# Optimization experiments

Hardware: AMD Instinct MI355X
Metric: run time of the kernel (lower is better)

## Reference

```python
import jax, jax.numpy as jnp
import numpy as np

AUTHOR_FAMILY_CODET = jnp.array([0, 1, 2, 1, 3, 3], dtype=jnp.int32)
MARGIN = 0.3

def setup_inputs() -> dict:
    key = jax.random.key(0)
    k1, k2 = jax.random.split(key)
    B, D = 8192, 256
    embeddings = jax.random.normal(k1, (B, D), dtype=jnp.float32)
    labels = jax.random.randint(k2, (B,), 0, 6, dtype=jnp.int64)
    return {"embeddings": embeddings, "labels": labels}

def reference(embeddings, labels):
    B = embeddings.shape[0]
    # family lookup; labels out of table range would be -1 (cannot happen here
    # since fill_max == table length, but kept for faithfulness)
    lab = labels.astype(jnp.int32)
    table_len = AUTHOR_FAMILY_CODET.shape[0]
    fam = jnp.where(lab < table_len,
                    AUTHOR_FAMILY_CODET[jnp.clip(lab, 0, table_len - 1)],
                    -1)
    # cosine distance matrix [B, B]
    emb_norm = embeddings / jnp.linalg.norm(embeddings, axis=-1, keepdims=True)
    dist = 1.0 - emb_norm @ emb_norm.T
    valid_row = fam >= 0                                   # [B]
    same = (fam[:, None] == fam[None, :]) & valid_row[:, None]
    same = same & ~jnp.eye(B, dtype=bool)                  # exclude self
    diff = (fam[:, None] != fam[None, :]) & valid_row[None, :] & valid_row[:, None]
    d_pos = jnp.max(jnp.where(same, dist, -2.0), axis=1)   # hardest positive
    d_neg = jnp.min(jnp.where(diff, dist, 4.0), axis=1)    # hardest negative
    valid = valid_row & jnp.any(same, axis=1) & jnp.any(diff, axis=1)
    triplet = jax.nn.relu(d_pos - d_neg + MARGIN) * valid.astype(dist.dtype)
    count = jnp.sum(valid.astype(jnp.int32))
    return jnp.sum(triplet) / jnp.maximum(count, 1).astype(dist.dtype)
```

## Files before the change

### kernel.cpp

```cpp
#include <hip/hip_runtime.h>


typedef __attribute__((ext_vector_type(8))) _Float16 half8;
typedef __attribute__((ext_vector_type(4))) float floatx4;
typedef __attribute__((ext_vector_type(4))) unsigned short ushort4v;

constexpr int D = 256;
#define MARGIN 0.3f
#define FAM_PACKED 111240

static __device__ __forceinline__ void ld_g2l16(const unsigned short* g,
                                                unsigned short* l) {
  __builtin_amdgcn_global_load_lds(
      (const __attribute__((address_space(1))) unsigned int*)(const void*)g,
      (__attribute__((address_space(3))) unsigned int*)(void*)l, 16, 0, 0);
}

static __device__ __forceinline__ unsigned packmm(float mn, float mx) {
  unsigned lo = __builtin_bit_cast(unsigned short, (_Float16)mn);
  unsigned hi = __builtin_bit_cast(unsigned short, (_Float16)mx);
  return lo | (hi << 16);
}
static __device__ __forceinline__ float mmlo(unsigned p) {
  return (float)__builtin_bit_cast(_Float16, (unsigned short)(p & 0xFFFF));
}
static __device__ __forceinline__ float mmhi(unsigned p) {
  return (float)__builtin_bit_cast(_Float16, (unsigned short)(p >> 16));
}

__global__ __launch_bounds__(256) void prep_kernel(
    const float* __restrict__ E, const int* __restrict__ labels,
    unsigned short* __restrict__ Eh, int* __restrict__ fam,
    float* __restrict__ sumAcc, int* __restrict__ cntAcc,
    int* __restrict__ doneCnt, int B) {
  if (blockIdx.x == 0 && threadIdx.x == 0) {
    sumAcc[0] = 0.0f; cntAcc[0] = 0; doneCnt[0] = 0;
  }
  int wave = blockIdx.x * 4 + (threadIdx.x >> 6);
  int lane = threadIdx.x & 63;
  int nw   = gridDim.x * 4;
  for (int row = wave; row < B; row += nw) {
    float4 v = *(const float4*)&E[(long)row * D + lane * 4];
    float s = v.x * v.x + v.y * v.y + v.z * v.z + v.w * v.w;
#pragma unroll
    for (int o = 1; o < 64; o <<= 1) s += __shfl_xor(s, o);
    float rn = 1.0f / sqrtf(s);
    ushort4v o4;
    o4.x = __builtin_bit_cast(unsigned short, (_Float16)(v.x * rn));
    o4.y = __builtin_bit_cast(unsigned short, (_Float16)(v.y * rn));
    o4.z = __builtin_bit_cast(unsigned short, (_Float16)(v.z * rn));
    o4.w = __builtin_bit_cast(unsigned short, (_Float16)(v.w * rn));
    *(ushort4v*)&Eh[(long)row * D + lane * 4] = o4;
    if (lane == 0) {
      int lab = labels[row];
      int labc = lab < 0 ? 0 : (lab > 5 ? 5 : lab);
      fam[row] = (lab < 6) ? ((FAM_PACKED >> (3 * labc)) & 7) : -1;
    }
  }
}

__global__ __launch_bounds__(256) void gram_kernel(
    const unsigned short* __restrict__ Eh, const int* __restrict__ fam,
    unsigned* __restrict__ part, int nt, int nTasks) {
  __shared__ unsigned short Bs[2][64 * 256];
  __shared__ unsigned colS[2][4][64];

  const int tid = threadIdx.x;
  const int w = tid >> 6, l = tid & 63;
  const int m = l & 15, q = l >> 4;
  const int half = w & 1;

  int srcRel[8];
#pragma unroll
  for (int t = 0; t < 8; ++t) {
    int c = w * 512 + t * 64 + l;
    int row = c >> 5, ch = c & 31;
    srcRel[t] = row * D + ((ch ^ (row & 7)) << 3);
  }

  const int t0 = (int)(((long)blockIdx.x * nTasks) / gridDim.x);
  const int t1 = (int)(((long)(blockIdx.x + 1) * nTasks) / gridDim.x);

  int rb = 0;
  while ((rb + 1) * (nt - rb) <= t0) ++rb;
  int ct = 2 * rb + (t0 - rb * (nt - rb + 1));

  half8 apan[8][2];
  int famv;
  {
    const int r0w = rb * 128 + w * 32;
#pragma unroll
    for (int ks = 0; ks < 8; ++ks)
#pragma unroll
      for (int mi = 0; mi < 2; ++mi)
        apan[ks][mi] = *(const half8*)
            &Eh[(long)(r0w + mi * 16 + m) * D + ks * 32 + q * 8];
    famv = fam[r0w + (l & 31)];
  }

  {
    const unsigned short* src = Eh + (long)ct * 64 * D;
#pragma unroll
    for (int t = 0; t < 8; ++t)
      ld_g2l16(src + srcRel[t], &Bs[0][(w * 512 + t * 64) * 8]);
  }

  int p = 0;
  int mct = -1, mrb = -1;
#pragma unroll 1
  for (int f = t0; f < t1; ++f) {
    __syncthreads();

    if (mct >= 0 && l < 16) {
      const int sb = (f - 1) & 1;
      const int col = w * 16 + l;
      float mn = 4.0f, mx = -4.0f;
#pragma unroll
      for (int ww = 0; ww < 4; ++ww) {
        unsigned pk = colS[sb][ww][col];
        mn = fminf(mn, mmlo(pk));
        mx = fmaxf(mx, mmhi(pk));
      }
      part[((long)mct * nt + mrb) * 64 + col] = packmm(mn, mx);
    }

    const int rt64 = 2 * rb + (w >> 1);
    const bool doit = (rt64 <= ct);
    const int sb = f & 1;
    floatx4 acc[2][4];
#pragma unroll
    for (int mi = 0; mi < 2; ++mi)
#pragma unroll
      for (int nj = 0; nj < 4; ++nj) acc[mi][nj] = (floatx4)0.0f;

    if (doit) {
      const unsigned short* bufp = &Bs[p][0];
#pragma unroll
      for (int ks = 0; ks < 8; ++ks) {
        half8 b[4];
#pragma unroll
        for (int nj = 0; nj < 4; ++nj) {
          int row = nj * 16 + m;
          b[nj] = *(const half8*)
              &bufp[row * 256 + (((ks * 4 + q) ^ (m & 7)) << 3)];
        }
#pragma unroll
        for (int mi = 0; mi < 2; ++mi)
#pragma unroll
          for (int nj = 0; nj < 4; ++nj)
            acc[mi][nj] = __builtin_amdgcn_mfma_f32_16x16x32_f16(
                apan[ks][mi], b[nj], acc[mi][nj], 0, 0, 0);
      }
    }

    int nrb = rb, nct = ct + 1;
    if (nct == nt) { ++nrb; nct = 2 * nrb; }
    if (f + 1 < t1) {
      const unsigned short* src = Eh + (long)nct * 64 * D;
#pragma unroll
      for (int t = 0; t < 8; ++t)
        ld_g2l16(src + srcRel[t], &Bs[p ^ 1][(w * 512 + t * 64) * 8]);
    }

    if (doit) {
      const int famcv = fam[ct * 64 + l];
      int famR[8], famC[4];
#pragma unroll
      for (int mi = 0; mi < 2; ++mi)
#pragma unroll
        for (int r = 0; r < 4; ++r)
          famR[mi * 4 + r] = __shfl(famv, mi * 16 + q * 4 + r);
#pragma unroll
      for (int nj = 0; nj < 4; ++nj) famC[nj] = __shfl(famcv, nj * 16 + m);

      float rMin[8], rMax[8], cMin[4], cMax[4];
#pragma unroll
      for (int i = 0; i < 8; ++i) { rMin[i] = 4.0f; rMax[i] = -4.0f; }
#pragma unroll
      for (int j = 0; j < 4; ++j) { cMin[j] = 4.0f; cMax[j] = -4.0f; }

#pragma unroll
      for (int mi = 0; mi < 2; ++mi)
#pragma unroll
        for (int nj = 0; nj < 4; ++nj)
#pragma unroll
          for (int r = 0; r < 4; ++r) {
            float d = acc[mi][nj][r];
            bool same = (famR[mi * 4 + r] == famC[nj]);
            float ds = same ? d : 4.0f;
            float dd = same ? -4.0f : d;
            rMin[mi * 4 + r] = fminf(rMin[mi * 4 + r], ds);
            rMax[mi * 4 + r] = fmaxf(rMax[mi * 4 + r], dd);
            cMin[nj] = fminf(cMin[nj], ds);
            cMax[nj] = fmaxf(cMax[nj], dd);
          }

#pragma unroll
      for (int o = 1; o < 16; o <<= 1)
#pragma unroll
        for (int i = 0; i < 8; ++i) {
          rMin[i] = fminf(rMin[i], __shfl_xor(rMin[i], o));
          rMax[i] = fmaxf(rMax[i], __shfl_xor(rMax[i], o));
        }
      if (m == 0) {
        unsigned* dst = part + ((long)rt64 * nt + ct) * 64;
#pragma unroll
        for (int mi = 0; mi < 2; ++mi)
#pragma unroll
          for (int r = 0; r < 4; ++r)
            dst[half * 32 + mi * 16 + q * 4 + r] =
                packmm(rMin[mi * 4 + r], rMax[mi * 4 + r]);
      }
#pragma unroll
      for (int o = 16; o < 64; o <<= 1)
#pragma unroll
        for (int j = 0; j < 4; ++j) {
          cMin[j] = fminf(cMin[j], __shfl_xor(cMin[j], o));
          cMax[j] = fmaxf(cMax[j], __shfl_xor(cMax[j], o));
        }
      if (q == 0) {
        const bool real = (rt64 < ct);
#pragma unroll
        for (int nj = 0; nj < 4; ++nj)
          colS[sb][w][nj * 16 + m] =
              real ? packmm(cMin[nj], cMax[nj]) : packmm(4.0f, -4.0f);
      }
    } else {
      if (q == 0)
#pragma unroll
        for (int nj = 0; nj < 4; ++nj)
          colS[sb][w][nj * 16 + m] = packmm(4.0f, -4.0f);
    }

    mct = ct; mrb = rb;
    if (f + 1 < t1 && nrb != rb) {
      const int r0w = nrb * 128 + w * 32;
#pragma unroll
      for (int ks = 0; ks < 8; ++ks)
#pragma unroll
        for (int mi = 0; mi < 2; ++mi)
          apan[ks][mi] = *(const half8*)
              &Eh[(long)(r0w + mi * 16 + m) * D + ks * 32 + q * 8];
      famv = fam[r0w + (l & 31)];
    }
    rb = nrb; ct = nct; p ^= 1;
  }
  __syncthreads();
  if (l < 16) {
    const int sb = (t1 - 1) & 1;
    const int col = w * 16 + l;
    float mn = 4.0f, mx = -4.0f;
#pragma unroll
    for (int ww = 0; ww < 4; ++ww) {
      unsigned pk = colS[sb][ww][col];
      mn = fminf(mn, mmlo(pk));
      mx = fmaxf(mx, mmhi(pk));
    }
    part[((long)mct * nt + mrb) * 64 + col] = packmm(mn, mx);
  }
}

__global__ __launch_bounds__(256) void reduce_kernel(
    const unsigned* __restrict__ part, float* __restrict__ sumAcc,
    int* __restrict__ cntAcc, int* __restrict__ doneCnt,
    float* __restrict__ out, int B, int nt) {
  int gid = blockIdx.x * 256 + threadIdx.x;
  int row = gid >> 2;
  int c   = gid & 3;
  int rt = row >> 6, rl = row & 63;
  const unsigned* base = part + ((long)rt * nt) * 64 + rl;
  float mn = 4.0f, mx = -4.0f;
  for (int k = rt + c; k < nt; k += 4) {
    unsigned pk = base[(long)k * 64];
    mn = fminf(mn, mmlo(pk));
    mx = fmaxf(mx, mmhi(pk));
  }
  if (rt >= 1) {
    int rbmax = rt >> 1;
    for (int k = c; k <= rbmax; k += 4) {
      unsigned pk = base[(long)k * 64];
      mn = fminf(mn, mmlo(pk));
      mx = fmaxf(mx, mmhi(pk));
    }
  }
#pragma unroll
  for (int o = 1; o < 4; o <<= 1) {
    mn = fminf(mn, __shfl_xor(mn, o));
    mx = fmaxf(mx, __shfl_xor(mx, o));
  }
  float loss = 0.0f;
  int cc = 0;
  if (c == 0 && mn < 3.0f && mx > -3.0f) {
    loss = fmaxf(mx - mn + MARGIN, 0.0f);
    cc = 1;
  }
#pragma unroll
  for (int o = 1; o < 64; o <<= 1) {
    loss += __shfl_xor(loss, o);
    cc   += __shfl_xor(cc, o);
  }
  __shared__ float ls[4];
  __shared__ int   cs[4];
  if ((threadIdx.x & 63) == 0) {
    ls[threadIdx.x >> 6] = loss;
    cs[threadIdx.x >> 6] = cc;
  }
  __syncthreads();
  if (threadIdx.x == 0) {
    atomicAdd(sumAcc, ls[0] + ls[1] + ls[2] + ls[3]);
    atomicAdd(cntAcc, cs[0] + cs[1] + cs[2] + cs[3]);
    __threadfence();
    int old = atomicAdd(doneCnt, 1);
    if (old == (int)gridDim.x - 1) {
      float S = atomicAdd(sumAcc, 0.0f);
      int   C = atomicAdd(cntAcc, 0);
      out[0] = S / (float)(C > 0 ? C : 1);
    }
  }
}

extern "C" void kernel_launch(void* const* d_in, const int* in_sizes, int n_in,
                              void* d_out, int out_size, void* d_ws, size_t ws_size,
                              hipStream_t stream) {
  const float* E      = (const float*)d_in[0];
  const int*   labels = (const int*)d_in[1];
  float*       out    = (float*)d_out;
  const int B  = in_sizes[1];
  const int nt = B / 64;
  const int RB = nt / 2;
  const int nTasks = RB * (nt - RB + 1);

  unsigned short* Eh = (unsigned short*)d_ws;
  int* fam           = (int*)(Eh + (size_t)B * D);
  unsigned* part     = (unsigned*)(fam + B);
  float* sumAcc      = (float*)(part + (size_t)nt * nt * 64);
  int* cntAcc        = (int*)(sumAcc + 1);
  int* doneCnt       = cntAcc + 1;

  prep_kernel<<<dim3(256), 256, 0, stream>>>(E, labels, Eh, fam,
                                             sumAcc, cntAcc, doneCnt, B);
  gram_kernel<<<dim3(512), 256, 0, stream>>>(Eh, fam, part, nt, nTasks);
  reduce_kernel<<<dim3(B * 4 / 256), 256, 0, stream>>>(part, sumAcc, cntAcc,
                                                       doneCnt, out, B, nt);
}
```

Measured before the change: 126.7 us.

## Fold family masking into the Gram GEMM via one-hot extra dims and widen tiles

Each normalized row gets 32 extra fp16 columns holding a scaled one-hot of its family. An extra MFMA step then shifts same-family dot products by a constant, so hardest positive and hardest negative become a plain min/max with no per-element family compare. Blocks grow to 512 threads over 256-row bands, and each block keeps its A panel for the whole task range instead of reloading it. Partial min/max values are merged with packed-half min on sign-flipped bits. This removes the fam loads, shuffles and selects from the epilogue, at the cost of a wider K dimension, a more complex offset encoding, and fp16 precision limits on the shifted values.

```diff
diff --git a/kernel.cpp b/kernel.cpp
--- a/kernel.cpp
+++ b/kernel.cpp
@@ -2,12 +2,15 @@
 
 
 typedef __attribute__((ext_vector_type(8))) _Float16 half8;
+typedef __attribute__((ext_vector_type(2))) _Float16 half2v;
 typedef __attribute__((ext_vector_type(4))) float floatx4;
 typedef __attribute__((ext_vector_type(4))) unsigned short ushort4v;
 
-constexpr int D = 256;
+constexpr int DIN = 256;
+constexpr int DK  = 288;
 #define MARGIN 0.3f
 #define FAM_PACKED 111240
+#define SENT 0xC4004400u
 
 static __device__ __forceinline__ void ld_g2l16(const unsigned short* g,
                                                 unsigned short* l) {
@@ -27,12 +30,16 @@
 static __device__ __forceinline__ float mmhi(unsigned p) {
   return (float)__builtin_bit_cast(_Float16, (unsigned short)(p >> 16));
 }
+static __device__ __forceinline__ unsigned pkmin(unsigned a, unsigned b) {
+  half2v x = __builtin_bit_cast(half2v, a);
+  half2v y = __builtin_bit_cast(half2v, b);
+  return __builtin_bit_cast(unsigned, __builtin_elementwise_min(x, y));
+}
 
 __global__ __launch_bounds__(256) void prep_kernel(
     const float* __restrict__ E, const int* __restrict__ labels,
-    unsigned short* __restrict__ Eh, int* __restrict__ fam,
-    float* __restrict__ sumAcc, int* __restrict__ cntAcc,
-    int* __restrict__ doneCnt, int B) {
+    unsigned short* __restrict__ Eh, float* __restrict__ sumAcc,
+    int* __restrict__ cntAcc, int* __restrict__ doneCnt, int B) {
   if (blockIdx.x == 0 && threadIdx.x == 0) {
     sumAcc[0] = 0.0f; cntAcc[0] = 0; doneCnt[0] = 0;
   }
@@ -40,7 +47,7 @@
   int lane = threadIdx.x & 63;
   int nw   = gridDim.x * 4;
   for (int row = wave; row < B; row += nw) {
-    float4 v = *(const float4*)&E[(long)row * D + lane * 4];
+    float4 v = *(const float4*)&E[(long)row * DIN + lane * 4];
     float s = v.x * v.x + v.y * v.y + v.z * v.z + v.w * v.w;
 #pragma unroll
     for (int o = 1; o < 64; o <<= 1) s += __shfl_xor(s, o);
@@ -50,81 +57,88 @@
     o4.y = __builtin_bit_cast(unsigned short, (_Float16)(v.y * rn));
     o4.z = __builtin_bit_cast(unsigned short, (_Float16)(v.z * rn));
     o4.w = __builtin_bit_cast(unsigned short, (_Float16)(v.w * rn));
-    *(ushort4v*)&Eh[(long)row * D + lane * 4] = o4;
-    if (lane == 0) {
-      int lab = labels[row];
-      int labc = lab < 0 ? 0 : (lab > 5 ? 5 : lab);
-      fam[row] = (lab < 6) ? ((FAM_PACKED >> (3 * labc)) & 7) : -1;
-    }
-  }
-}
-
-__global__ __launch_bounds__(256) void gram_kernel(
-    const unsigned short* __restrict__ Eh, const int* __restrict__ fam,
-    unsigned* __restrict__ part, int nt, int nTasks) {
-  __shared__ unsigned short Bs[2][64 * 256];
-  __shared__ unsigned colS[2][4][64];
+    *(ushort4v*)&Eh[(long)row * DK + lane * 4] = o4;
+    if (lane < 8) {
+      ushort4v z = {0, 0, 0, 0};
+      if (lane == 0) {
+        int lab = labels[row];
+        int labc = lab < 0 ? 0 : (lab > 5 ? 5 : lab);
+        int fm = (FAM_PACKED >> (3 * labc)) & 7;
+        z.x = fm == 0 ? 0x4400 : 0;
+        z.y = fm == 1 ? 0x4400 : 0;
+        z.z = fm == 2 ? 0x4400 : 0;
+        z.w = fm == 3 ? 0x4400 : 0;
+      }
+      *(ushort4v*)&Eh[(long)row * DK + DIN + lane * 4] = z;
+    }
+  }
+}
+
+__global__ __launch_bounds__(512, 4) void gram_kernel(
+    const unsigned short* __restrict__ Eh, unsigned* __restrict__ part,
+    int nt, int nTasks) {
+  __shared__ unsigned short Bs[2][64 * DK];
+  __shared__ unsigned colS[2][8][64];
 
   const int tid = threadIdx.x;
   const int w = tid >> 6, l = tid & 63;
   const int m = l & 15, q = l >> 4;
   const int half = w & 1;
-
-  int srcRel[8];
-#pragma unroll
-  for (int t = 0; t < 8; ++t) {
-    int c = w * 512 + t * 64 + l;
-    int row = c >> 5, ch = c & 31;
-    srcRel[t] = row * D + ((ch ^ (row & 7)) << 3);
+  const int m7 = l & 7;
+
+  int srcRel[5];
+#pragma unroll
+  for (int t = 0; t < 5; ++t) {
+    int c = (t < 4) ? (t * 512 + w * 64 + l) : (2048 + w * 64 + l);
+    int row = c / 36, ch = c - row * 36;
+    int sch = (ch < 32) ? (ch ^ (row & 7)) : ch;
+    srcRel[t] = row * DK + sch * 8;
   }
 
   const int t0 = (int)(((long)blockIdx.x * nTasks) / gridDim.x);
   const int t1 = (int)(((long)(blockIdx.x + 1) * nTasks) / gridDim.x);
 
   int rb = 0;
-  while ((rb + 1) * (nt - rb) <= t0) ++rb;
-  int ct = 2 * rb + (t0 - rb * (nt - rb + 1));
+  while ((rb + 1) * (nt - 2 * rb) <= t0) ++rb;
+  int ct = 4 * rb + (t0 - rb * (nt - 2 * (rb - 1)));
+
+  const int rt64 = 4 * rb + (w >> 1);
 
   half8 apan[8][2];
-  int famv;
   {
-    const int r0w = rb * 128 + w * 32;
+    const int r0w = rb * 256 + w * 32;
 #pragma unroll
     for (int ks = 0; ks < 8; ++ks)
 #pragma unroll
       for (int mi = 0; mi < 2; ++mi)
         apan[ks][mi] = *(const half8*)
-            &Eh[(long)(r0w + mi * 16 + m) * D + ks * 32 + q * 8];
-    famv = fam[r0w + (l & 31)];
-  }
+            &Eh[(long)(r0w + mi * 16 + m) * DK + ks * 32 + q * 8];
+  }
+  const int aextOff = (rb * 256 + w * 32 + m) * DK + DIN + q * 8;
 
   {
-    const unsigned short* src = Eh + (long)ct * 64 * D;
-#pragma unroll
-    for (int t = 0; t < 8; ++t)
-      ld_g2l16(src + srcRel[t], &Bs[0][(w * 512 + t * 64) * 8]);
-  }
-
-  int p = 0;
-  int mct = -1, mrb = -1;
+    const unsigned short* src = Eh + (long)ct * 64 * DK;
+#pragma unroll
+    for (int t = 0; t < 4; ++t)
+      ld_g2l16(src + srcRel[t], &Bs[0][(t * 512 + w * 64) * 8]);
+    if (w < 4) ld_g2l16(src + srcRel[4], &Bs[0][(2048 + w * 64) * 8]);
+  }
+
+  int p = 0, mct = -1;
 #pragma unroll 1
   for (int f = t0; f < t1; ++f) {
     __syncthreads();
 
-    if (mct >= 0 && l < 16) {
-      const int sb = (f - 1) & 1;
-      const int col = w * 16 + l;
-      float mn = 4.0f, mx = -4.0f;
-#pragma unroll
-      for (int ww = 0; ww < 4; ++ww) {
-        unsigned pk = colS[sb][ww][col];
-        mn = fminf(mn, mmlo(pk));
-        mx = fmaxf(mx, mmhi(pk));
-      }
-      part[((long)mct * nt + mrb) * 64 + col] = packmm(mn, mx);
-    }
-
-    const int rt64 = 2 * rb + (w >> 1);
+    if (mct > 4 * rb && l < 8) {
+      const int sb2 = (f - 1) & 1;
+      const int col = w * 8 + l;
+      unsigned a = SENT ^ 0x80000000u;
+#pragma unroll
+      for (int ww = 0; ww < 8; ++ww)
+        a = pkmin(a, colS[sb2][ww][col] ^ 0x80000000u);
+      part[((long)mct * nt + rb) * 64 + col] = a ^ 0x80000000u;
+    }
+
     const bool doit = (rt64 <= ct);
     const int sb = f & 1;
     floatx4 acc[2][4];
@@ -135,15 +149,31 @@
 
     if (doit) {
       const unsigned short* bufp = &Bs[p][0];
+      {
+        half8 ae[2];
+#pragma unroll
+        for (int mi = 0; mi < 2; ++mi) {
+          ae[mi] = *(const half8*)&Eh[(long)(aextOff + mi * 16 * DK)];
+          ae[mi] = ae[mi] * (_Float16)-0.5f;
+        }
+        half8 b[4];
+#pragma unroll
+        for (int nj = 0; nj < 4; ++nj)
+          b[nj] = *(const half8*)&bufp[(nj * 16 + m) * DK + (32 + q) * 8];
+#pragma unroll
+        for (int mi = 0; mi < 2; ++mi)
+#pragma unroll
+          for (int nj = 0; nj < 4; ++nj)
+            acc[mi][nj] = __builtin_amdgcn_mfma_f32_16x16x32_f16(
+                ae[mi], b[nj], acc[mi][nj], 0, 0, 0);
+      }
 #pragma unroll
       for (int ks = 0; ks < 8; ++ks) {
         half8 b[4];
 #pragma unroll
-        for (int nj = 0; nj < 4; ++nj) {
-          int row = nj * 16 + m;
+        for (int nj = 0; nj < 4; ++nj)
           b[nj] = *(const half8*)
-              &bufp[row * 256 + (((ks * 4 + q) ^ (m & 7)) << 3)];
-        }
+              &bufp[(nj * 16 + m) * DK + (((ks * 4 + q) ^ m7) << 3)];
 #pragma unroll
         for (int mi = 0; mi < 2; ++mi)
 #pragma unroll
@@ -153,55 +183,48 @@
       }
     }
 
-    int nrb = rb, nct = ct + 1;
-    if (nct == nt) { ++nrb; nct = 2 * nrb; }
     if (f + 1 < t1) {
-      const unsigned short* src = Eh + (long)nct * 64 * D;
-#pragma unroll
-      for (int t = 0; t < 8; ++t)
-        ld_g2l16(src + srcRel[t], &Bs[p ^ 1][(w * 512 + t * 64) * 8]);
+      const unsigned short* src = Eh + (long)(ct + 1) * 64 * DK;
+#pragma unroll
+      for (int t = 0; t < 4; ++t)
+        ld_g2l16(src + srcRel[t], &Bs[p ^ 1][(t * 512 + w * 64) * 8]);
+      if (w < 4) ld_g2l16(src + srcRel[4], &Bs[p ^ 1][(2048 + w * 64) * 8]);
     }
 
     if (doit) {
-      const int famcv = fam[ct * 64 + l];
-      int famR[8], famC[4];
-#pragma unroll
-      for (int mi = 0; mi < 2; ++mi)
-#pragma unroll
-        for (int r = 0; r < 4; ++r)
-          famR[mi * 4 + r] = __shfl(famv, mi * 16 + q * 4 + r);
-#pragma unroll
-      for (int nj = 0; nj < 4; ++nj) famC[nj] = __shfl(famcv, nj * 16 + m);
-
-      float rMin[8], rMax[8], cMin[4], cMax[4];
-#pragma unroll
-      for (int i = 0; i < 8; ++i) { rMin[i] = 4.0f; rMax[i] = -4.0f; }
-#pragma unroll
-      for (int j = 0; j < 4; ++j) { cMin[j] = 4.0f; cMax[j] = -4.0f; }
-
-#pragma unroll
-      for (int mi = 0; mi < 2; ++mi)
-#pragma unroll
-        for (int nj = 0; nj < 4; ++nj)
+      float rMn[8], rMx[8];
+#pragma unroll
+      for (int i = 0; i < 8; ++i) { rMn[i] = 4.0f; rMx[i] = -4.0f; }
+      unsigned cPk[4];
+#pragma unroll
+      for (int nj = 0; nj < 4; ++nj) {
+        float cmn = 4.0f, cmx = -4.0f;
+#pragma unroll
+        for (int mi = 0; mi < 2; ++mi) {
+          floatx4 vv = acc[mi][nj];
 #pragma unroll
           for (int r = 0; r < 4; ++r) {
-            float d = acc[mi][nj][r];
-            bool same = (famR[mi * 4 + r] == famC[nj]);
-            float ds = same ? d : 4.0f;
-            float dd = same ? -4.0f : d;
-            rMin[mi * 4 + r] = fminf(rMin[mi * 4 + r], ds);
-            rMax[mi * 4 + r] = fmaxf(rMax[mi * 4 + r], dd);
-            cMin[nj] = fminf(cMin[nj], ds);
-            cMax[nj] = fmaxf(cMax[nj], dd);
+            rMn[mi * 4 + r] = fminf(rMn[mi * 4 + r], vv[r]);
+            rMx[mi * 4 + r] = fmaxf(rMx[mi * 4 + r], vv[r]);
           }
-
+          cmn = fminf(cmn, fminf(fminf(vv[0], vv[1]), fminf(vv[2], vv[3])));
+          cmx = fmaxf(cmx, fmaxf(fmaxf(vv[0], vv[1]), fmaxf(vv[2], vv[3])));
+        }
+        unsigned cp = packmm(cmn + 8.0f, cmx) ^ 0x80000000u;
+        cp = pkmin(cp, __shfl_xor(cp, 16));
+        cp = pkmin(cp, __shfl_xor(cp, 32));
+        cPk[nj] = cp;
+      }
+
+      unsigned rp[8];
+#pragma unroll
+      for (int i = 0; i < 8; ++i)
+        rp[i] = packmm(rMn[i] + 8.0f, rMx[i]) ^ 0x80000000u;
 #pragma unroll
       for (int o = 1; o < 16; o <<= 1)
 #pragma unroll
-        for (int i = 0; i < 8; ++i) {
-          rMin[i] = fminf(rMin[i], __shfl_xor(rMin[i], o));
-          rMax[i] = fmaxf(rMax[i], __shfl_xor(rMax[i], o));
-        }
+        for (int i = 0; i < 8; ++i)
+          rp[i] = pkmin(rp[i], __shfl_xor(rp[i], o));
       if (m == 0) {
         unsigned* dst = part + ((long)rt64 * nt + ct) * 64;
 #pragma unroll
@@ -209,54 +232,32 @@
 #pragma unroll
           for (int r = 0; r < 4; ++r)
             dst[half * 32 + mi * 16 + q * 4 + r] =
-                packmm(rMin[mi * 4 + r], rMax[mi * 4 + r]);
-      }
-#pragma unroll
-      for (int o = 16; o < 64; o <<= 1)
-#pragma unroll
-        for (int j = 0; j < 4; ++j) {
-          cMin[j] = fminf(cMin[j], __shfl_xor(cMin[j], o));
-          cMax[j] = fmaxf(cMax[j], __shfl_xor(cMax[j], o));
-        }
+                rp[mi * 4 + r] ^ 0x80000000u;
+      }
       if (q == 0) {
         const bool real = (rt64 < ct);
 #pragma unroll
         for (int nj = 0; nj < 4; ++nj)
-          colS[sb][w][nj * 16 + m] =
-              real ? packmm(cMin[nj], cMax[nj]) : packmm(4.0f, -4.0f);
+          colS[sb][w][nj * 16 + m] = real ? (cPk[nj] ^ 0x80000000u) : SENT;
       }
     } else {
       if (q == 0)
 #pragma unroll
-        for (int nj = 0; nj < 4; ++nj)
-          colS[sb][w][nj * 16 + m] = packmm(4.0f, -4.0f);
-    }
-
-    mct = ct; mrb = rb;
-    if (f + 1 < t1 && nrb != rb) {
-      const int r0w = nrb * 128 + w * 32;
-#pragma unroll
-      for (int ks = 0; ks < 8; ++ks)
-#pragma unroll
-        for (int mi = 0; mi < 2; ++mi)
-          apan[ks][mi] = *(const half8*)
-              &Eh[(long)(r0w + mi * 16 + m) * D + ks * 32 + q * 8];
-      famv = fam[r0w + (l & 31)];
-    }
-    rb = nrb; ct = nct; p ^= 1;
-  }
+        for (int nj = 0; nj < 4; ++nj) colS[sb][w][nj * 16 + m] = SENT;
+    }
+
+    mct = ct; ++ct; p ^= 1;
+  }
+
   __syncthreads();
-  if (l < 16) {
-    const int sb = (t1 - 1) & 1;
-    const int col = w * 16 + l;
-    float mn = 4.0f, mx = -4.0f;
-#pragma unroll
-    for (int ww = 0; ww < 4; ++ww) {
-      unsigned pk = colS[sb][ww][col];
-      mn = fminf(mn, mmlo(pk));
-      mx = fmaxf(mx, mmhi(pk));
-    }
-    part[((long)mct * nt + mrb) * 64 + col] = packmm(mn, mx);
+  if (mct > 4 * rb && l < 8) {
+    const int sb2 = (t1 - 1) & 1;
+    const int col = w * 8 + l;
+    unsigned a = SENT ^ 0x80000000u;
+#pragma unroll
+    for (int ww = 0; ww < 8; ++ww)
+      a = pkmin(a, colS[sb2][ww][col] ^ 0x80000000u);
+    part[((long)mct * nt + rb) * 64 + col] = a ^ 0x80000000u;
   }
 }
 
@@ -276,7 +277,7 @@
     mx = fmaxf(mx, mmhi(pk));
   }
   if (rt >= 1) {
-    int rbmax = rt >> 1;
+    int rbmax = (rt - 1) >> 2;
     for (int k = c; k <= rbmax; k += 4) {
       unsigned pk = base[(long)k * 64];
       mn = fminf(mn, mmlo(pk));
@@ -327,19 +328,18 @@
   float*       out    = (float*)d_out;
   const int B  = in_sizes[1];
   const int nt = B / 64;
-  const int RB = nt / 2;
-  const int nTasks = RB * (nt - RB + 1);
+  const int RB = B / 256;
+  const int nTasks = RB * (nt - 2 * (RB - 1));
 
   unsigned short* Eh = (unsigned short*)d_ws;
-  int* fam           = (int*)(Eh + (size_t)B * D);
-  unsigned* part     = (unsigned*)(fam + B);
+  unsigned* part     = (unsigned*)(Eh + (size_t)B * DK);
   float* sumAcc      = (float*)(part + (size_t)nt * nt * 64);
   int* cntAcc        = (int*)(sumAcc + 1);
   int* doneCnt       = cntAcc + 1;
 
-  prep_kernel<<<dim3(256), 256, 0, stream>>>(E, labels, Eh, fam,
+  prep_kernel<<<dim3(256), 256, 0, stream>>>(E, labels, Eh,
                                              sumAcc, cntAcc, doneCnt, B);
-  gram_kernel<<<dim3(512), 256, 0, stream>>>(Eh, fam, part, nt, nTasks);
+  gram_kernel<<<dim3(nTasks / 4), 512, 0, stream>>>(Eh, part, nt, nTasks);
   reduce_kernel<<<dim3(B * 4 / 256), 256, 0, stream>>>(part, sumAcc, cntAcc,
                                                        doneCnt, out, B, nt);
 }
```

New measurement: 144.5 us. +14.0%, slower.
